# Performance work log

Measured on AMD Instinct MI355X. Metric: run time of the kernel, lower is better.

The kernel has to match this reference:

```python
import jax, jax.numpy as jnp
import numpy as np


def ray_sampler(cam2world, intrinsics, resolution):
    # EG3D RaySampler: pixel centers in [0,1], lifted through intrinsics, rotated to world.
    B = cam2world.shape[0]
    fx = intrinsics[:, 0, 0][:, None]
    fy = intrinsics[:, 1, 1][:, None]
    cx = intrinsics[:, 0, 2][:, None]
    cy = intrinsics[:, 1, 2][:, None]
    sk = intrinsics[:, 0, 1][:, None]
    ii, jj = jnp.meshgrid(jnp.arange(resolution), jnp.arange(resolution), indexing='ij')
    # torch.meshgrid + flip(0): x = column index, y = row index (row-major flatten)
    x = ((jj.reshape(-1).astype(jnp.float32) + 0.5) / resolution)[None, :]  # [1, M]
    y = ((ii.reshape(-1).astype(jnp.float32) + 0.5) / resolution)[None, :]  # [1, M]
    x_lift = (x - cx + cy * sk / fy - sk * y / fy) / fx        # [B, M]
    y_lift = (y - cy) / fy                                     # [B, M]
    ones = jnp.ones_like(x_lift)
    cam_rel = jnp.stack([x_lift, y_lift, ones, ones], axis=-1)  # [B, M, 4]
    world = jnp.einsum('bij,bmj->bmi', cam2world, cam_rel)[..., :3]  # [B, M, 3]
    cam_loc = cam2world[:, :3, 3]                               # [B, 3]
    dirs = world - cam_loc[:, None, :]
    dirs = dirs / jnp.maximum(jnp.linalg.norm(dirs, axis=-1, keepdims=True), 1e-12)
    origins = jnp.broadcast_to(cam_loc[:, None, :], dirs.shape)
    return origins, dirs


def setup_inputs() -> dict:
    key = jax.random.key(0)
    k1, k2, k3 = jax.random.split(key, 3)
    B, res, N = 4, 128, 2048
    # realistic camera: identity rotation, camera near z=2.7 (EG3D radius), normalized intrinsics
    t = jnp.concatenate([0.05 * jax.random.normal(k1, (B, 2)), jnp.full((B, 1), 2.7)], axis=1)
    c2w = jnp.tile(jnp.eye(4, dtype=jnp.float32)[None], (B, 1, 1)).at[:, :3, 3].set(t)
    intr = jnp.tile(jnp.array([[4.2647, 0.0, 0.5], [0.0, 4.2647, 0.5], [0.0, 0.0, 1.0]],
                              dtype=jnp.float32)[None], (B, 1, 1))
    c = jnp.concatenate([c2w.reshape(B, 16), intr.reshape(B, 9)], axis=1)  # [B, 25]
    image_depth = 2.2 + jax.random.uniform(k2, (B, 1, res, res), dtype=jnp.float32)
    pc = 0.3 * jax.random.normal(k3, (B, N, 3), dtype=jnp.float32)
    return {"c": c, "image_depth": image_depth, "pc": pc, "neural_rendering_resolution": 128}


def reference(c, image_depth, pc, neural_rendering_resolution):
    B = c.shape[0]
    res = neural_rendering_resolution
    M = res * res
    cam2world = c[:, :16].reshape(B, 4, 4)
    intrinsics = c[:, 16:25].reshape(B, 3, 3)
    ray_origins, ray_dirs = ray_sampler(cam2world, intrinsics, res)  # [B, M, 3] each
    pc3 = pc[..., :3]                                                # [B, N, 3]
    # distance from camera origin to every pc point -> max per sample
    d0 = jnp.linalg.norm(ray_origins[:, :1, :] - pc3, axis=-1)       # [B, N]
    max_distance = jnp.max(d0, axis=1)                               # [B]
    depth = image_depth.reshape(B, M, 1)
    pred = depth * ray_dirs + ray_origins                            # [B, M, 3]
    mask = depth.reshape(B, M) < max_distance[:, None]               # [B, M]
    # chamfer dist1 (direction=0): squared distance of each pred point to nearest pc point
    d2 = (jnp.sum(pred * pred, axis=-1)[:, :, None]
          + jnp.sum(pc3 * pc3, axis=-1)[:, None, :]
          - 2.0 * jnp.einsum('bmd,bnd->bmn', pred, pc3))             # [B, M, N]
    min_d2 = jnp.maximum(jnp.min(d2, axis=2), 0.0)                   # [B, M]
    # ragged masked mean == mean over pred_[mask_] in the original loop
    m = mask.astype(min_d2.dtype)
    loss = jnp.sum(min_d2 * m, axis=1) / jnp.maximum(jnp.sum(m, axis=1), 1.0)
    return loss.reshape(B, 1)
```

## Files before the change

kernel.cpp:

```cpp
#include <hip/hip_runtime.h>
#include <math.h>

#define TPB 512
#define WAVES 8
#define RAYS_PB 256
#define RPT 4
#define MAXPTS 2048

__global__ __launch_bounds__(TPB) void chamfer_main(
    const float* __restrict__ c, const float* __restrict__ depth,
    const float* __restrict__ pc, float2* __restrict__ partial,
    int res, int M, int N)
{
    __shared__ float4 spts[MAXPTS];
    __shared__ float red[WAVES][RAYS_PB];
    __shared__ float smax[WAVES];
    __shared__ float bs[RPT], bc[RPT];

    int tile = blockIdx.x, b = blockIdx.y;
    int tid = threadIdx.x, w = tid >> 6, lane = tid & 63;

    const float* cb = c + b * 25;
    float fx = cb[16], sk = cb[17], cx = cb[18];
    float fy = cb[20], cy = cb[21];
    float ox = cb[3], oy = cb[7], oz = cb[11];

    float px[RPT], py[RPT], pz[RPT], pn[RPT], dep[RPT], mxs[RPT];
    #pragma unroll
    for (int r = 0; r < RPT; ++r) {
        int m = tile * RAYS_PB + lane + 64 * r;
        int mm = min(m, M - 1);
        int i = mm / res, j = mm - i * res;
        float x = (j + 0.5f) / (float)res;
        float y = (i + 0.5f) / (float)res;
        float xl = (x - cx + cy * sk / fy - sk * y / fy) / fx;
        float yl = (y - cy) / fy;
        float wx = cb[0] * xl + cb[1] * yl + cb[2] + cb[3];
        float wy = cb[4] * xl + cb[5] * yl + cb[6] + cb[7];
        float wz = cb[8] * xl + cb[9] * yl + cb[10] + cb[11];
        float dx = wx - ox, dy = wy - oy, dz = wz - oz;
        float nrm = fmaxf(sqrtf(dx * dx + dy * dy + dz * dz), 1e-12f);
        dx /= nrm; dy /= nrm; dz /= nrm;
        float d = depth[(size_t)b * M + mm];
        dep[r] = d;
        px[r] = fmaf(d, dx, ox);
        py[r] = fmaf(d, dy, oy);
        pz[r] = fmaf(d, dz, oz);
        pn[r] = px[r] * px[r] + py[r] * py[r] + pz[r] * pz[r];
        mxs[r] = -3.4e38f;
    }

    float mdl = 0.0f;
    for (int n0 = 0; n0 < N; n0 += MAXPTS) {
        int kc = min(N - n0, MAXPTS);
        if (n0) __syncthreads();
        const float* src = pc + ((size_t)b * N + n0) * 3;
        for (int p = tid; p < kc; p += TPB) {
            float qx = src[3 * p], qy = src[3 * p + 1], qz = src[3 * p + 2];
            float qn = qx * qx + qy * qy + qz * qz;
            spts[p] = make_float4(qx, qy, qz, -0.5f * qn);
            float dx = qx - ox, dy = qy - oy, dz = qz - oz;
            mdl = fmaxf(mdl, dx * dx + dy * dy + dz * dz);
        }
        __syncthreads();

        int cpw = (kc + WAVES - 1) / WAVES;
        int s0 = min(w * cpw, kc);
        int s1 = min(s0 + cpw, kc);
        #pragma unroll 8
        for (int k = s0; k < s1; ++k) {
            float4 q = spts[k];
            #pragma unroll
            for (int r = 0; r < RPT; ++r) {
                float s = fmaf(pz[r], q.z, q.w);
                s = fmaf(py[r], q.y, s);
                s = fmaf(px[r], q.x, s);
                mxs[r] = fmaxf(mxs[r], s);
            }
        }
    }

    for (int off = 32; off; off >>= 1) mdl = fmaxf(mdl, __shfl_down(mdl, off));
    if (lane == 0) smax[w] = mdl;
    #pragma unroll
    for (int r = 0; r < RPT; ++r) red[w][lane + 64 * r] = mxs[r];
    __syncthreads();

    float s = 0.f, cnt = 0.f;
    if (tid < RAYS_PB) {
        float m2 = smax[0];
        #pragma unroll
        for (int ww = 1; ww < WAVES; ++ww) m2 = fmaxf(m2, smax[ww]);
        float thr = sqrtf(m2);

        float mx = red[0][tid];
        #pragma unroll
        for (int ww = 1; ww < WAVES; ++ww) mx = fmaxf(mx, red[ww][tid]);
        float pnk = pn[0], dk = dep[0];
        #pragma unroll
        for (int r = 1; r < RPT; ++r) if (w == r) { pnk = pn[r]; dk = dep[r]; }
        int m = tile * RAYS_PB + tid;
        if (m < M) {
            float md = fmaxf(fmaf(-2.0f, mx, pnk), 0.0f);
            if (dk < thr) { s = md; cnt = 1.0f; }
        }
    }
    for (int off = 32; off; off >>= 1) {
        s += __shfl_down(s, off);
        cnt += __shfl_down(cnt, off);
    }
    if (tid < RAYS_PB && lane == 0) { bs[w] = s; bc[w] = cnt; }
    __syncthreads();
    if (tid == 0) {
        float S = 0.f, C = 0.f;
        #pragma unroll
        for (int ww = 0; ww < RPT; ++ww) { S += bs[ww]; C += bc[ww]; }
        partial[(size_t)b * gridDim.x + blockIdx.x] = make_float2(S, C);
    }
}

__global__ __launch_bounds__(1024) void finalize_kernel(
    const float2* __restrict__ partial, float* __restrict__ out,
    int ntiles, int B)
{
    int w = threadIdx.x >> 6, lane = threadIdx.x & 63;
    if (w >= B) return;
    float S = 0.f, C = 0.f;
    for (int i = lane; i < ntiles; i += 64) {
        float2 p = partial[(size_t)w * ntiles + i];
        S += p.x; C += p.y;
    }
    for (int off = 32; off; off >>= 1) {
        S += __shfl_down(S, off);
        C += __shfl_down(C, off);
    }
    if (lane == 0) out[w] = S / fmaxf(C, 1.0f);
}

extern "C" void kernel_launch(void* const* d_in, const int* in_sizes, int n_in,
                              void* d_out, int out_size, void* d_ws, size_t ws_size,
                              hipStream_t stream) {
    const float* c     = (const float*)d_in[0];
    const float* depth = (const float*)d_in[1];
    const float* pc    = (const float*)d_in[2];

    int B = in_sizes[0] / 25;
    int M = in_sizes[1] / B;
    int N = in_sizes[2] / (3 * B);
    int res = 1;
    while (res * res < M) ++res;

    float2* partial = (float2*)d_ws;

    int ntiles = (M + RAYS_PB - 1) / RAYS_PB;

    chamfer_main<<<dim3(ntiles, B), TPB, 0, stream>>>(c, depth, pc, partial,
                                                      res, M, N);
    finalize_kernel<<<1, B * 64, 0, stream>>>(partial, (float*)d_out,
                                              ntiles, B);
}
```

Measured before the change: 21.82 us.

## Use packed fp16 dot2 for chamfer inner loop with half-precision point storage

```diff
diff --git a/kernel.cpp b/kernel.cpp
--- a/kernel.cpp
+++ b/kernel.cpp
@@ -7,12 +7,29 @@
 #define RPT 4
 #define MAXPTS 2048
 
+typedef _Float16 h2 __attribute__((ext_vector_type(2)));
+
+__device__ __forceinline__ h2 bch2(unsigned int u) {
+    union { unsigned int u; h2 h; } v; v.u = u; return v.h;
+}
+__device__ __forceinline__ unsigned int bcu(h2 h) {
+    union { h2 h; unsigned int u; } v; v.h = h; return v.u;
+}
+
+__device__ __forceinline__ float dot2acc(h2 a, h2 b, float c) {
+#if __has_builtin(__builtin_amdgcn_fdot2)
+    return __builtin_amdgcn_fdot2(a, b, c, false);
+#else
+    return fmaf((float)a[0], (float)b[0], fmaf((float)a[1], (float)b[1], c));
+#endif
+}
+
 __global__ __launch_bounds__(TPB) void chamfer_main(
     const float* __restrict__ c, const float* __restrict__ depth,
     const float* __restrict__ pc, float2* __restrict__ partial,
     int res, int M, int N)
 {
-    __shared__ float4 spts[MAXPTS];
+    __shared__ uint4 spair[MAXPTS / 2];
     __shared__ float red[WAVES][RAYS_PB];
     __shared__ float smax[WAVES];
     __shared__ float bs[RPT], bc[RPT];
@@ -25,7 +42,8 @@
     float fy = cb[20], cy = cb[21];
     float ox = cb[3], oy = cb[7], oz = cb[11];
 
-    float px[RPT], py[RPT], pz[RPT], pn[RPT], dep[RPT], mxs[RPT];
+    h2 pxy[RPT], pz1[RPT];
+    float pn[RPT], dep[RPT], mxs[RPT];
     #pragma unroll
     for (int r = 0; r < RPT; ++r) {
         int m = tile * RAYS_PB + lane + 64 * r;
@@ -43,10 +61,12 @@
         dx /= nrm; dy /= nrm; dz /= nrm;
         float d = depth[(size_t)b * M + mm];
         dep[r] = d;
-        px[r] = fmaf(d, dx, ox);
-        py[r] = fmaf(d, dy, oy);
-        pz[r] = fmaf(d, dz, oz);
-        pn[r] = px[r] * px[r] + py[r] * py[r] + pz[r] * pz[r];
+        float px_ = fmaf(d, dx, ox);
+        float py_ = fmaf(d, dy, oy);
+        float pz_ = fmaf(d, dz, oz);
+        pn[r] = px_ * px_ + py_ * py_ + pz_ * pz_;
+        pxy[r] = (h2){(_Float16)px_, (_Float16)py_};
+        pz1[r] = (h2){(_Float16)pz_, (_Float16)1.0f};
         mxs[r] = -3.4e38f;
     }
 
@@ -55,27 +75,73 @@
         int kc = min(N - n0, MAXPTS);
         if (n0) __syncthreads();
         const float* src = pc + ((size_t)b * N + n0) * 3;
-        for (int p = tid; p < kc; p += TPB) {
+
+        int g4 = kc >> 2;
+        const float4* s4 = (const float4*)src;
+        for (int g = tid; g < g4; g += TPB) {
+            float4 f0 = s4[3 * g], f1 = s4[3 * g + 1], f2 = s4[3 * g + 2];
+            float qx0 = f0.x, qy0 = f0.y, qz0 = f0.z;
+            float qx1 = f0.w, qy1 = f1.x, qz1 = f1.y;
+            float qx2 = f1.z, qy2 = f1.w, qz2 = f2.x;
+            float qx3 = f2.y, qy3 = f2.z, qz3 = f2.w;
+            float qn0 = qx0*qx0 + qy0*qy0 + qz0*qz0;
+            float qn1 = qx1*qx1 + qy1*qy1 + qz1*qz1;
+            float qn2 = qx2*qx2 + qy2*qy2 + qz2*qz2;
+            float qn3 = qx3*qx3 + qy3*qy3 + qz3*qz3;
+            uint4 e0, e1;
+            e0.x = bcu((h2){(_Float16)qx0, (_Float16)qy0});
+            e0.y = bcu((h2){(_Float16)qz0, (_Float16)(-0.5f * qn0)});
+            e0.z = bcu((h2){(_Float16)qx1, (_Float16)qy1});
+            e0.w = bcu((h2){(_Float16)qz1, (_Float16)(-0.5f * qn1)});
+            e1.x = bcu((h2){(_Float16)qx2, (_Float16)qy2});
+            e1.y = bcu((h2){(_Float16)qz2, (_Float16)(-0.5f * qn2)});
+            e1.z = bcu((h2){(_Float16)qx3, (_Float16)qy3});
+            e1.w = bcu((h2){(_Float16)qz3, (_Float16)(-0.5f * qn3)});
+            spair[2 * g]     = e0;
+            spair[2 * g + 1] = e1;
+            float d0x = qx0 - ox, d0y = qy0 - oy, d0z = qz0 - oz;
+            float d1x = qx1 - ox, d1y = qy1 - oy, d1z = qz1 - oz;
+            float d2x = qx2 - ox, d2y = qy2 - oy, d2z = qz2 - oz;
+            float d3x = qx3 - ox, d3y = qy3 - oy, d3z = qz3 - oz;
+            mdl = fmaxf(mdl, fmaxf(
+                fmaxf(d0x*d0x + d0y*d0y + d0z*d0z, d1x*d1x + d1y*d1y + d1z*d1z),
+                fmaxf(d2x*d2x + d2y*d2y + d2z*d2z, d3x*d3x + d3y*d3y + d3z*d3z)));
+        }
+        for (int p = (g4 << 2) + tid; p < kc; p += TPB) {
             float qx = src[3 * p], qy = src[3 * p + 1], qz = src[3 * p + 2];
             float qn = qx * qx + qy * qy + qz * qz;
-            spts[p] = make_float4(qx, qy, qz, -0.5f * qn);
+            uint2 e;
+            e.x = bcu((h2){(_Float16)qx, (_Float16)qy});
+            e.y = bcu((h2){(_Float16)qz, (_Float16)(-0.5f * qn)});
+            ((uint2*)spair)[p] = e;
             float dx = qx - ox, dy = qy - oy, dz = qz - oz;
             mdl = fmaxf(mdl, dx * dx + dy * dy + dz * dz);
         }
         __syncthreads();
 
-        int cpw = (kc + WAVES - 1) / WAVES;
+        int cpw = (((kc >> 1) + WAVES - 1) / WAVES) << 1;
         int s0 = min(w * cpw, kc);
         int s1 = min(s0 + cpw, kc);
-        #pragma unroll 8
-        for (int k = s0; k < s1; ++k) {
-            float4 q = spts[k];
+        int pp0 = s0 >> 1, pp1 = s1 >> 1;
+        #pragma unroll 4
+        for (int kk = pp0; kk < pp1; ++kk) {
+            uint4 qq = spair[kk];
+            h2 a0 = bch2(qq.x), a1 = bch2(qq.y);
+            h2 b0 = bch2(qq.z), b1 = bch2(qq.w);
             #pragma unroll
             for (int r = 0; r < RPT; ++r) {
-                float s = fmaf(pz[r], q.z, q.w);
-                s = fmaf(py[r], q.y, s);
-                s = fmaf(px[r], q.x, s);
-                mxs[r] = fmaxf(mxs[r], s);
+                float sa = dot2acc(pz1[r], a1, dot2acc(pxy[r], a0, 0.0f));
+                float sb = dot2acc(pz1[r], b1, dot2acc(pxy[r], b0, 0.0f));
+                mxs[r] = fmaxf(mxs[r], fmaxf(sa, sb));
+            }
+        }
+        if ((s1 & 1) && s1 == kc) {
+            uint2 qv = ((const uint2*)spair)[kc - 1];
+            h2 a0 = bch2(qv.x), a1 = bch2(qv.y);
+            #pragma unroll
+            for (int r = 0; r < RPT; ++r) {
+                float sa = dot2acc(pz1[r], a1, dot2acc(pxy[r], a0, 0.0f));
+                mxs[r] = fmaxf(mxs[r], sa);
             }
         }
     }
```

New measurement: 26.59 us. +21.9%, slower.

## Broadcast point cloud via readlane registers instead of LDS staging

Applied to the files above, without the earlier changes.

```diff
diff --git a/kernel.cpp b/kernel.cpp
--- a/kernel.cpp
+++ b/kernel.cpp
@@ -5,17 +5,20 @@
 #define WAVES 8
 #define RAYS_PB 256
 #define RPT 4
-#define MAXPTS 2048
+#define PPL 4
+
+__device__ __forceinline__ float rl(float v, int g) {
+    return __int_as_float(__builtin_amdgcn_readlane(__float_as_int(v), g));
+}
 
 __global__ __launch_bounds__(TPB) void chamfer_main(
     const float* __restrict__ c, const float* __restrict__ depth,
     const float* __restrict__ pc, float2* __restrict__ partial,
     int res, int M, int N)
 {
-    __shared__ float4 spts[MAXPTS];
     __shared__ float red[WAVES][RAYS_PB];
     __shared__ float smax[WAVES];
-    __shared__ float bs[RPT], bc[RPT];
+    __shared__ float bs[RAYS_PB / 64], bc[RAYS_PB / 64];
 
     int tile = blockIdx.x, b = blockIdx.y;
     int tid = threadIdx.x, w = tid >> 6, lane = tid & 63;
@@ -50,32 +53,67 @@
         mxs[r] = -3.4e38f;
     }
 
+    const float* pcb = pc + (size_t)b * N * 3;
     float mdl = 0.0f;
-    for (int n0 = 0; n0 < N; n0 += MAXPTS) {
-        int kc = min(N - n0, MAXPTS);
-        if (n0) __syncthreads();
-        const float* src = pc + ((size_t)b * N + n0) * 3;
-        for (int p = tid; p < kc; p += TPB) {
-            float qx = src[3 * p], qy = src[3 * p + 1], qz = src[3 * p + 2];
-            float qn = qx * qx + qy * qy + qz * qz;
-            spts[p] = make_float4(qx, qy, qz, -0.5f * qn);
-            float dx = qx - ox, dy = qy - oy, dz = qz - oz;
-            mdl = fmaxf(mdl, dx * dx + dy * dy + dz * dz);
+    const int SWEEP = WAVES * 64 * PPL;
+    for (int n0 = 0; n0 < N; n0 += SWEEP) {
+        int idx0 = n0 + (w * 64 + lane) * PPL;
+        float4 qa, qb, qc, qd;
+        if (idx0 + PPL <= N) {
+            const float4* s4 = (const float4*)(pcb + (size_t)idx0 * 3);
+            float4 f0 = s4[0], f1 = s4[1], f2 = s4[2];
+            qa = make_float4(f0.x, f0.y, f0.z, 0.f);
+            qb = make_float4(f0.w, f1.x, f1.y, 0.f);
+            qc = make_float4(f1.z, f1.w, f2.x, 0.f);
+            qd = make_float4(f2.y, f2.z, f2.w, 0.f);
+        } else {
+            int i0 = min(idx0,     N - 1) * 3;
+            int i1 = min(idx0 + 1, N - 1) * 3;
+            int i2 = min(idx0 + 2, N - 1) * 3;
+            int i3 = min(idx0 + 3, N - 1) * 3;
+            qa = make_float4(pcb[i0], pcb[i0 + 1], pcb[i0 + 2], 0.f);
+            qb = make_float4(pcb[i1], pcb[i1 + 1], pcb[i1 + 2], 0.f);
+            qc = make_float4(pcb[i2], pcb[i2 + 1], pcb[i2 + 2], 0.f);
+            qd = make_float4(pcb[i3], pcb[i3 + 1], pcb[i3 + 2], 0.f);
         }
-        __syncthreads();
+        qa.w = -0.5f * (qa.x * qa.x + qa.y * qa.y + qa.z * qa.z);
+        qb.w = -0.5f * (qb.x * qb.x + qb.y * qb.y + qb.z * qb.z);
+        qc.w = -0.5f * (qc.x * qc.x + qc.y * qc.y + qc.z * qc.z);
+        qd.w = -0.5f * (qd.x * qd.x + qd.y * qd.y + qd.z * qd.z);
+        {
+            float ax = qa.x - ox, ay = qa.y - oy, az = qa.z - oz;
+            float bx = qb.x - ox, by = qb.y - oy, bz = qb.z - oz;
+            float cx2 = qc.x - ox, cy2 = qc.y - oy, cz2 = qc.z - oz;
+            float dx2 = qd.x - ox, dy2 = qd.y - oy, dz2 = qd.z - oz;
+            mdl = fmaxf(mdl, fmaxf(
+                fmaxf(ax*ax + ay*ay + az*az, bx*bx + by*by + bz*bz),
+                fmaxf(cx2*cx2 + cy2*cy2 + cz2*cz2, dx2*dx2 + dy2*dy2 + dz2*dz2)));
+        }
 
-        int cpw = (kc + WAVES - 1) / WAVES;
-        int s0 = min(w * cpw, kc);
-        int s1 = min(s0 + cpw, kc);
-        #pragma unroll 8
-        for (int k = s0; k < s1; ++k) {
-            float4 q = spts[k];
-            #pragma unroll
-            for (int r = 0; r < RPT; ++r) {
-                float s = fmaf(pz[r], q.z, q.w);
-                s = fmaf(py[r], q.y, s);
-                s = fmaf(px[r], q.x, s);
-                mxs[r] = fmaxf(mxs[r], s);
+        for (int g = 0; g < 64; ++g) {
+            {
+                float axv = rl(qa.x, g), ayv = rl(qa.y, g);
+                float azv = rl(qa.z, g), awv = rl(qa.w, g);
+                float bxv = rl(qb.x, g), byv = rl(qb.y, g);
+                float bzv = rl(qb.z, g), bwv = rl(qb.w, g);
+                #pragma unroll
+                for (int r = 0; r < RPT; ++r) {
+                    float sa = fmaf(px[r], axv, fmaf(py[r], ayv, fmaf(pz[r], azv, awv)));
+                    float sb = fmaf(px[r], bxv, fmaf(py[r], byv, fmaf(pz[r], bzv, bwv)));
+                    mxs[r] = fmaxf(mxs[r], fmaxf(sa, sb));
+                }
+            }
+            {
+                float axv = rl(qc.x, g), ayv = rl(qc.y, g);
+                float azv = rl(qc.z, g), awv = rl(qc.w, g);
+                float bxv = rl(qd.x, g), byv = rl(qd.y, g);
+                float bzv = rl(qd.z, g), bwv = rl(qd.w, g);
+                #pragma unroll
+                for (int r = 0; r < RPT; ++r) {
+                    float sa = fmaf(px[r], axv, fmaf(py[r], ayv, fmaf(pz[r], azv, awv)));
+                    float sb = fmaf(px[r], bxv, fmaf(py[r], byv, fmaf(pz[r], bzv, bwv)));
+                    mxs[r] = fmaxf(mxs[r], fmaxf(sa, sb));
+                }
             }
         }
     }
@@ -114,7 +152,7 @@
     if (tid == 0) {
         float S = 0.f, C = 0.f;
         #pragma unroll
-        for (int ww = 0; ww < RPT; ++ww) { S += bs[ww]; C += bc[ww]; }
+        for (int ww = 0; ww < RAYS_PB / 64; ++ww) { S += bs[ww]; C += bc[ww]; }
         partial[(size_t)b * gridDim.x + blockIdx.x] = make_float2(S, C);
     }
 }
```

New measurement: 32.40 us. +48.5%, slower.

## Compute ray-to-point dot products with bf16 MFMA instead of FP32 FMAs

Applied to the files above, without the earlier changes.

```diff
diff --git a/kernel.cpp b/kernel.cpp
--- a/kernel.cpp
+++ b/kernel.cpp
@@ -4,31 +4,41 @@
 #define TPB 512
 #define WAVES 8
 #define RAYS_PB 256
-#define RPT 4
 #define MAXPTS 2048
+#define PTILE 32
+
+typedef short short8 __attribute__((ext_vector_type(8)));
+typedef float f32x16 __attribute__((ext_vector_type(16)));
+
+__device__ __forceinline__ unsigned int f2bf(float f) {
+    unsigned int u = __float_as_uint(f);
+    u += 0x7FFFu + ((u >> 16) & 1u);
+    return u >> 16;
+}
 
 __global__ __launch_bounds__(TPB) void chamfer_main(
     const float* __restrict__ c, const float* __restrict__ depth,
     const float* __restrict__ pc, float2* __restrict__ partial,
     int res, int M, int N)
 {
-    __shared__ float4 spts[MAXPTS];
-    __shared__ float red[WAVES][RAYS_PB];
+    __shared__ uint2 spts[MAXPTS];
+    __shared__ float redR[WAVES][32][33];
+    __shared__ float pnL[RAYS_PB], depL[RAYS_PB];
     __shared__ float smax[WAVES];
-    __shared__ float bs[RPT], bc[RPT];
+    __shared__ float bs[4], bc[4];
 
     int tile = blockIdx.x, b = blockIdx.y;
     int tid = threadIdx.x, w = tid >> 6, lane = tid & 63;
+    int colb = lane & 31, hh = lane >> 5;
 
     const float* cb = c + b * 25;
     float fx = cb[16], sk = cb[17], cx = cb[18];
     float fy = cb[20], cy = cb[21];
     float ox = cb[3], oy = cb[7], oz = cb[11];
 
-    float px[RPT], py[RPT], pz[RPT], pn[RPT], dep[RPT], mxs[RPT];
-    #pragma unroll
-    for (int r = 0; r < RPT; ++r) {
-        int m = tile * RAYS_PB + lane + 64 * r;
+    short8 afrag = {0, 0, 0, 0, 0, 0, 0, 0};
+    {
+        int m = tile * RAYS_PB + w * 32 + colb;
         int mm = min(m, M - 1);
         int i = mm / res, j = mm - i * res;
         float x = (j + 0.5f) / (float)res;
@@ -42,48 +52,89 @@
         float nrm = fmaxf(sqrtf(dx * dx + dy * dy + dz * dz), 1e-12f);
         dx /= nrm; dy /= nrm; dz /= nrm;
         float d = depth[(size_t)b * M + mm];
-        dep[r] = d;
-        px[r] = fmaf(d, dx, ox);
-        py[r] = fmaf(d, dy, oy);
-        pz[r] = fmaf(d, dz, oz);
-        pn[r] = px[r] * px[r] + py[r] * py[r] + pz[r] * pz[r];
-        mxs[r] = -3.4e38f;
-    }
+        float px_ = fmaf(d, dx, ox);
+        float py_ = fmaf(d, dy, oy);
+        float pz_ = fmaf(d, dz, oz);
+        float pn_ = px_ * px_ + py_ * py_ + pz_ * pz_;
+        if (hh == 0) {
+            pnL[w * 32 + colb] = pn_;
+            depL[w * 32 + colb] = d;
+            afrag[0] = (short)f2bf(px_);
+            afrag[1] = (short)f2bf(py_);
+            afrag[2] = (short)f2bf(pz_);
+            afrag[3] = (short)0x3F80;
+        }
+    }
+
+    const f32x16 zacc = {0.f,0.f,0.f,0.f,0.f,0.f,0.f,0.f,
+                         0.f,0.f,0.f,0.f,0.f,0.f,0.f,0.f};
+    float mx[16];
+    #pragma unroll
+    for (int r = 0; r < 16; ++r) mx[r] = -3.4e38f;
 
     float mdl = 0.0f;
     for (int n0 = 0; n0 < N; n0 += MAXPTS) {
         int kc = min(N - n0, MAXPTS);
+        int kcp = ((kc + PTILE - 1) / PTILE) * PTILE;
         if (n0) __syncthreads();
         const float* src = pc + ((size_t)b * N + n0) * 3;
-        for (int p = tid; p < kc; p += TPB) {
-            float qx = src[3 * p], qy = src[3 * p + 1], qz = src[3 * p + 2];
-            float qn = qx * qx + qy * qy + qz * qz;
-            spts[p] = make_float4(qx, qy, qz, -0.5f * qn);
+
+        int g4 = kc >> 2;
+        const float4* s4 = (const float4*)src;
+        for (int g = tid; g < g4; g += TPB) {
+            float4 f0 = s4[3 * g], f1 = s4[3 * g + 1], f2 = s4[3 * g + 2];
+            float qx0 = f0.x, qy0 = f0.y, qz0 = f0.z;
+            float qx1 = f0.w, qy1 = f1.x, qz1 = f1.y;
+            float qx2 = f1.z, qy2 = f1.w, qz2 = f2.x;
+            float qx3 = f2.y, qy3 = f2.z, qz3 = f2.w;
+            float w0 = -0.5f * (qx0*qx0 + qy0*qy0 + qz0*qz0);
+            float w1 = -0.5f * (qx1*qx1 + qy1*qy1 + qz1*qz1);
+            float w2 = -0.5f * (qx2*qx2 + qy2*qy2 + qz2*qz2);
+            float w3 = -0.5f * (qx3*qx3 + qy3*qy3 + qz3*qz3);
+            spts[4*g+0] = make_uint2(f2bf(qx0) | (f2bf(qy0) << 16), f2bf(qz0) | (f2bf(w0) << 16));
+            spts[4*g+1] = make_uint2(f2bf(qx1) | (f2bf(qy1) << 16), f2bf(qz1) | (f2bf(w1) << 16));
+            spts[4*g+2] = make_uint2(f2bf(qx2) | (f2bf(qy2) << 16), f2bf(qz2) | (f2bf(w2) << 16));
+            spts[4*g+3] = make_uint2(f2bf(qx3) | (f2bf(qy3) << 16), f2bf(qz3) | (f2bf(w3) << 16));
+            float a0 = qx0 - ox, a1 = qy0 - oy, a2 = qz0 - oz;
+            float b0 = qx1 - ox, b1 = qy1 - oy, b2 = qz1 - oz;
+            float c0 = qx2 - ox, c1 = qy2 - oy, c2 = qz2 - oz;
+            float d0 = qx3 - ox, d1 = qy3 - oy, d2 = qz3 - oz;
+            mdl = fmaxf(mdl, fmaxf(
+                fmaxf(a0*a0 + a1*a1 + a2*a2, b0*b0 + b1*b1 + b2*b2),
+                fmaxf(c0*c0 + c1*c1 + c2*c2, d0*d0 + d1*d1 + d2*d2)));
+        }
+        for (int p = (g4 << 2) + tid; p < kc; p += TPB) {
+            float qx = src[3*p], qy = src[3*p+1], qz = src[3*p+2];
+            float qn = qx*qx + qy*qy + qz*qz;
+            spts[p] = make_uint2(f2bf(qx) | (f2bf(qy) << 16),
+                                 f2bf(qz) | (f2bf(-0.5f * qn) << 16));
             float dx = qx - ox, dy = qy - oy, dz = qz - oz;
-            mdl = fmaxf(mdl, dx * dx + dy * dy + dz * dz);
-        }
+            mdl = fmaxf(mdl, dx*dx + dy*dy + dz*dz);
+        }
+        for (int p = kc + tid; p < kcp; p += TPB)
+            spts[p] = make_uint2(0u, 0xC61C0000u);
         __syncthreads();
 
-        int cpw = (kc + WAVES - 1) / WAVES;
-        int s0 = min(w * cpw, kc);
-        int s1 = min(s0 + cpw, kc);
-        #pragma unroll 8
-        for (int k = s0; k < s1; ++k) {
-            float4 q = spts[k];
+        int ntt = kcp >> 5;
+        #pragma unroll 2
+        for (int t = 0; t < ntt; ++t) {
+            uint2 qv = spts[t * 32 + colb];
+            union { uint4 u; short8 s; } bu;
+            bu.u = make_uint4(qv.x, qv.y, 0u, 0u);
+            f32x16 dacc = __builtin_amdgcn_mfma_f32_32x32x16_bf16(
+                afrag, bu.s, zacc, 0, 0, 0);
             #pragma unroll
-            for (int r = 0; r < RPT; ++r) {
-                float s = fmaf(pz[r], q.z, q.w);
-                s = fmaf(py[r], q.y, s);
-                s = fmaf(px[r], q.x, s);
-                mxs[r] = fmaxf(mxs[r], s);
-            }
+            for (int r = 0; r < 16; ++r) mx[r] = fmaxf(mx[r], dacc[r]);
         }
     }
 
     for (int off = 32; off; off >>= 1) mdl = fmaxf(mdl, __shfl_down(mdl, off));
     if (lane == 0) smax[w] = mdl;
     #pragma unroll
-    for (int r = 0; r < RPT; ++r) red[w][lane + 64 * r] = mxs[r];
+    for (int r = 0; r < 16; ++r) {
+        int row = (r & 3) + 8 * (r >> 2) + 4 * hh;
+        redR[w][row][colb] = mx[r];
+    }
     __syncthreads();
 
     float s = 0.f, cnt = 0.f;
@@ -93,16 +144,15 @@
         for (int ww = 1; ww < WAVES; ++ww) m2 = fmaxf(m2, smax[ww]);
         float thr = sqrtf(m2);
 
-        float mx = red[0][tid];
+        int w2 = tid >> 5, row = tid & 31;
+        float mxx = redR[w2][row][0];
         #pragma unroll
-        for (int ww = 1; ww < WAVES; ++ww) mx = fmaxf(mx, red[ww][tid]);
-        float pnk = pn[0], dk = dep[0];
-        #pragma unroll
-        for (int r = 1; r < RPT; ++r) if (w == r) { pnk = pn[r]; dk = dep[r]; }
-        int m = tile * RAYS_PB + tid;
-        if (m < M) {
-            float md = fmaxf(fmaf(-2.0f, mx, pnk), 0.0f);
-            if (dk < thr) { s = md; cnt = 1.0f; }
+        for (int col = 1; col < 32; ++col) mxx = fmaxf(mxx, redR[w2][row][col]);
+
+        int mray = tile * RAYS_PB + tid;
+        if (mray < M) {
+            float md = fmaxf(fmaf(-2.0f, mxx, pnL[tid]), 0.0f);
+            if (depL[tid] < thr) { s = md; cnt = 1.0f; }
         }
     }
     for (int off = 32; off; off >>= 1) {
@@ -114,7 +164,7 @@
     if (tid == 0) {
         float S = 0.f, C = 0.f;
         #pragma unroll
-        for (int ww = 0; ww < RPT; ++ww) { S += bs[ww]; C += bc[ww]; }
+        for (int ww = 0; ww < 4; ++ww) { S += bs[ww]; C += bc[ww]; }
         partial[(size_t)b * gridDim.x + blockIdx.x] = make_float2(S, C);
     }
 }
@@ -151,7 +201,6 @@
     while (res * res < M) ++res;
 
     float2* partial = (float2*)d_ws;
-
     int ntiles = (M + RAYS_PB - 1) / RAYS_PB;
 
     chamfer_main<<<dim3(ntiles, B), TPB, 0, stream>>>(c, depth, pc, partial,
```

New measurement: 23.11 us. 5.9% more time.
